# Kernel optimization log

Measured on AMD Instinct MI355X. Metric: run time of the kernel, lower is better.

The kernel has to match this reference:

```python
import jax, jax.numpy as jnp
import numpy as np

EPS = 1e-5

def _layernorm(x, g, b):
    mu = jnp.mean(x, axis=-1, keepdims=True)
    var = jnp.mean(jnp.square(x - mu), axis=-1, keepdims=True)
    return (x - mu) * jax.lax.rsqrt(var + EPS) * g + b

def setup_inputs() -> dict:
    key = jax.random.key(0)
    ks = jax.random.split(key, 12)
    B, S, D, F = 2, 2048, 1024, 4096
    w = lambda k, shp: jax.random.normal(k, shp, dtype=jnp.float32) * 0.02
    return {
        "x":  jax.random.normal(ks[0], (B, S, D), dtype=jnp.float32),
        "Wq": w(ks[1], (D, D)), "bq": jnp.zeros((D,), jnp.float32),
        "Wk": w(ks[2], (D, D)), "bk": jnp.zeros((D,), jnp.float32),
        "Wv": w(ks[3], (D, D)), "bv": jnp.zeros((D,), jnp.float32),
        "W1": w(ks[4], (F, D)), "b1": jnp.zeros((F,), jnp.float32),
        "W2": w(ks[5], (D, F)), "b2": jnp.zeros((D,), jnp.float32),
        "g1": jnp.ones((D,), jnp.float32), "beta1": jnp.zeros((D,), jnp.float32),
        "g2": jnp.ones((D,), jnp.float32), "beta2": jnp.zeros((D,), jnp.float32),
    }

def reference(x, Wq, bq, Wk, bk, Wv, bv, W1, b1, W2, b2, g1, beta1, g2, beta2):
    B, S, D = x.shape
    H = 16
    dk = D // H
    # QKV projections (torch nn.Linear: y = x @ W.T + b)
    q = (x @ Wq.T + bq).reshape(B, S, H, dk).transpose(0, 2, 1, 3)  # [B,H,S,dk]
    k = (x @ Wk.T + bk).reshape(B, S, H, dk).transpose(0, 2, 1, 3)
    v = (x @ Wv.T + bv).reshape(B, S, H, dk).transpose(0, 2, 1, 3)
    # naive full attention (no mask, dropout=identity in eval)
    scores = jnp.einsum("bhqd,bhkd->bhqk", q, k) / jnp.sqrt(jnp.float32(dk))
    probs = jax.nn.softmax(scores, axis=-1)
    attn = jnp.einsum("bhqk,bhkd->bhqd", probs, v)  # [B,H,S,dk]
    attn_out = attn.transpose(0, 2, 1, 3).reshape(B, S, D)  # NOTE: no output proj (combine unused in source)
    # residual + LN1
    h = _layernorm(x + attn_out, g1, beta1)
    # FFN: linear2(relu(linear1(h)))
    ffn = jax.nn.relu(h @ W1.T + b1) @ W2.T + b2
    # residual + LN2
    return _layernorm(h + ffn, g2, beta2)
```

## Files before the change

### kernel.cpp

```cpp
#include <hip/hip_runtime.h>
#include <stdint.h>

typedef unsigned short u16;
typedef __bf16 bf16x8 __attribute__((ext_vector_type(8)));
typedef short s16x8 __attribute__((ext_vector_type(8)));
typedef float f32x4 __attribute__((ext_vector_type(4)));

union FragU { s16x8 s; bf16x8 b; uint4 u; };

__device__ __forceinline__ f32x4 mfma_bf16(s16x8 a, s16x8 b, f32x4 c) {
    FragU ua, ub; ua.s = a; ub.s = b;
    return __builtin_amdgcn_mfma_f32_16x16x32_bf16(ua.b, ub.b, c, 0, 0, 0);
}

__device__ __forceinline__ u16 f2bf(float f) {
    uint32_t u = __float_as_uint(f);
    u += 0x7fffu + ((u >> 16) & 1u);
    return (u16)(u >> 16);
}

__device__ __forceinline__ float bf2f(u16 u) {
    return __uint_as_float((uint32_t)u << 16);
}

__device__ __forceinline__ void gload_lds16(const void* g, void* l) {
    __builtin_amdgcn_global_load_lds((__attribute__((address_space(1))) void*)g,
                                     (__attribute__((address_space(3))) void*)l,
                                     16, 0, 0);
}

__device__ __forceinline__ void xcd_swz(int& bx, int& by, int& bz) {
    int nx = gridDim.x, ny = gridDim.y;
    int nwg = nx * ny * gridDim.z;
    int lin = blockIdx.x + nx * (blockIdx.y + ny * blockIdx.z);
    int cpx = nwg >> 3;
    int s = (lin & 7) * cpx + (lin >> 3);
    bx = s % nx; s /= nx;
    by = s % ny; bz = s / ny;
}

__global__ void k_cast(const float* __restrict__ in, u16* __restrict__ out, int n4) {
    int i = blockIdx.x * blockDim.x + threadIdx.x;
    int stride = gridDim.x * blockDim.x;
    for (; i < n4; i += stride) {
        float4 v = ((const float4*)in)[i];
        u16 us[4] = {f2bf(v.x), f2bf(v.y), f2bf(v.z), f2bf(v.w)};
        *(uint2*)(out + (size_t)i * 4) = *(uint2*)us;
    }
}

template<int RELU, int OUTMODE>
__device__ __forceinline__ void gemm_body(
    const u16* __restrict__ A, const u16* __restrict__ W,
    const float* __restrict__ bias, void* __restrict__ Cout,
    int M, int N, int K, int row0, int col0, int kbeg, int kend)
{
    __shared__ __align__(16) u16 As[128 * 64];
    __shared__ __align__(16) u16 Bs[128 * 64];

    const int tid  = threadIdx.x;
    const int wid  = tid >> 6;
    const int lane = tid & 63;
    const int g    = lane >> 4;
    const int cc   = lane & 15;
    const int wr   = wid >> 1;
    const int wc   = wid & 1;

    f32x4 zero = {0.f, 0.f, 0.f, 0.f};
    f32x4 acc[4][4];
#pragma unroll
    for (int i = 0; i < 4; i++)
#pragma unroll
        for (int j = 0; j < 4; j++) acc[i][j] = zero;

    const int srow = tid >> 3;
    const int scol = ((tid & 7) ^ (srow & 7)) * 8;
    const u16* gA0 = A + (size_t)(row0 + srow) * K + scol;
    const u16* gB0 = W + (size_t)(col0 + srow) * K + scol;
    u16* lA0 = &As[wid * 512];
    u16* lB0 = &Bs[wid * 512];

    const int xm = (cc & 7);

    for (int k0 = kbeg; k0 < kend; k0 += 64) {
#pragma unroll
        for (int j = 0; j < 4; j++)
            gload_lds16(gA0 + (size_t)(j * 32) * K + k0, lA0 + j * 2048);
#pragma unroll
        for (int j = 0; j < 4; j++)
            gload_lds16(gB0 + (size_t)(j * 32) * K + k0, lB0 + j * 2048);
        __syncthreads();

#pragma unroll
        for (int h = 0; h < 2; h++) {
            const int slot = ((h * 4 + g) ^ xm) * 8;
            s16x8 af[4], bf[4];
#pragma unroll
            for (int mi = 0; mi < 4; mi++)
                af[mi] = *(const s16x8*)&As[(wr * 64 + mi * 16 + cc) * 64 + slot];
#pragma unroll
            for (int ni = 0; ni < 4; ni++)
                bf[ni] = *(const s16x8*)&Bs[(wc * 64 + ni * 16 + cc) * 64 + slot];
#pragma unroll
            for (int mi = 0; mi < 4; mi++)
#pragma unroll
                for (int ni = 0; ni < 4; ni++)
                    acc[mi][ni] = mfma_bf16(af[mi], bf[ni], acc[mi][ni]);
        }
        __syncthreads();
    }

#pragma unroll
    for (int ni = 0; ni < 4; ni++) {
        int col = col0 + wc * 64 + ni * 16 + cc;
        float bvv = 0.f;
        if (OUTMODE != 2) bvv = bias[col];
        if (OUTMODE == 3) {
            int head = col >> 6, dh = col & 63;
#pragma unroll
            for (int mi = 0; mi < 4; mi++) {
                int row = row0 + wr * 64 + mi * 16 + g * 4;
                int bb = row >> 11, sl = row & 2047;
                u16 us[4];
#pragma unroll
                for (int r = 0; r < 4; r++) us[r] = f2bf(acc[mi][ni][r] + bvv);
                *(uint2*)&((u16*)Cout)[(((size_t)(bb * 16 + head) * 64 + dh) << 11) + sl]
                    = *(uint2*)us;
            }
        } else {
#pragma unroll
            for (int mi = 0; mi < 4; mi++) {
                int row = row0 + wr * 64 + mi * 16 + g * 4;
#pragma unroll
                for (int r = 0; r < 4; r++) {
                    float v = acc[mi][ni][r] + bvv;
                    if (RELU) v = fmaxf(v, 0.f);
                    size_t idx = (size_t)(row + r) * N + col;
                    if (OUTMODE == 0) ((float*)Cout)[idx] = v;
                    else              ((u16*)Cout)[idx] = f2bf(v);
                }
            }
        }
    }
}

__global__ __launch_bounds__(256, 4) void k_gemm_qk(
    const u16* __restrict__ A, const u16* __restrict__ Wq, const u16* __restrict__ Wk,
    const float* __restrict__ bq, const float* __restrict__ bk,
    u16* __restrict__ Q, u16* __restrict__ K, int M, int N, int Kd)
{
    int bx, by, bz; xcd_swz(bx, by, bz);
    const u16* W = (bz == 0) ? Wq : Wk;
    const float* bb = (bz == 0) ? bq : bk;
    u16* out = (bz == 0) ? Q : K;
    gemm_body<0, 1>(A, W, bb, out, M, N, Kd, by * 128, bx * 128, 0, Kd);
}

__global__ __launch_bounds__(256, 4) void k_gemm_vT(
    const u16* __restrict__ A, const u16* __restrict__ Wv, const float* __restrict__ bv,
    u16* __restrict__ Vt, int M, int N, int Kd)
{
    int bx, by, bz; xcd_swz(bx, by, bz);
    gemm_body<0, 3>(A, Wv, bv, Vt, M, N, Kd, by * 128, bx * 128, 0, Kd);
}

__global__ __launch_bounds__(256, 4) void k_gemm_relu_bf16(
    const u16* __restrict__ A, const u16* __restrict__ W, const float* __restrict__ bias,
    u16* __restrict__ C, int M, int N, int K)
{
    int bx, by, bz; xcd_swz(bx, by, bz);
    gemm_body<1, 1>(A, W, bias, C, M, N, K, by * 128, bx * 128, 0, K);
}

__global__ __launch_bounds__(256, 4) void k_gemm_part(
    const u16* __restrict__ A, const u16* __restrict__ W,
    u16* __restrict__ p0, u16* __restrict__ p1, u16* __restrict__ p2, u16* __restrict__ p3,
    int M, int N, int K)
{
    int bx, by, bz; xcd_swz(bx, by, bz);
    u16* out = (bz == 0) ? p0 : (bz == 1) ? p1 : (bz == 2) ? p2 : p3;
    gemm_body<0, 2>(A, W, nullptr, out, M, N, K, by * 128, bx * 128, bz * 1024, bz * 1024 + 1024);
}

__global__ __launch_bounds__(512, 4) void k_flash(
    const u16* __restrict__ Q, const u16* __restrict__ Kb,
    const u16* __restrict__ Vt, float* __restrict__ O)
{
    constexpr int S = 2048, Dm = 1024, H = 16;
    constexpr int KVB = 128;
    constexpr float qsc = 0.125f * 1.44269504f;
    int bx, by, bz; xcd_swz(bx, by, bz);
    int qt = bx, h = by, b = bz;
    int tid = threadIdx.x, wid = tid >> 6, lane = tid & 63;
    int g = lane >> 4, cc = lane & 15;

    __shared__ __align__(16) u16 Ks[128 * 64];
    __shared__ __align__(16) u16 Vs[64 * 128];

    int q0 = qt * 128 + wid * 16;
    size_t base = (size_t)b * S * Dm + h * 64;

    FragU uq0, uq1, qs0, qs1;
    uq0.s = *(const s16x8*)(Q + base + (size_t)(q0 + cc) * Dm + g * 8);
    uq1.s = *(const s16x8*)(Q + base + (size_t)(q0 + cc) * Dm + 32 + g * 8);
#pragma unroll
    for (int e = 0; e < 8; e++) {
        qs0.b[e] = (__bf16)((float)uq0.b[e] * qsc);
        qs1.b[e] = (__bf16)((float)uq1.b[e] * qsc);
    }
    s16x8 qf0 = qs0.s, qf1 = qs1.s;

    f32x4 minit = {-8.f, -8.f, -8.f, -8.f};
    f32x4 zero = {0.f, 0.f, 0.f, 0.f};
    f32x4 o[4];
#pragma unroll
    for (int t = 0; t < 4; t++) o[t] = zero;
    f32x4 lacc = zero;

    const int krow = tid >> 3;
    const int kcol = ((tid & 7) ^ (krow & 7)) * 8;
    const u16* kSrcBase = Kb + base + (size_t)krow * Dm + kcol;
    u16* kDst0 = &Ks[wid * 512];
    u16* kDst1 = kDst0 + 4096;

    const int vrow = tid >> 3;
    const int vch  = (tid & 7) * 8;
    const int xmv  = (vrow & 7) << 3;
    const int cb0  = ((vch >> 5) << 5) | (((vch >> 4) & 1) << 2) | (((vch >> 2) & 3) << 3);
    const int cb1  = cb0 + 64;
    const u16* vSrcBase = Vt + (size_t)(b * H + h) * 64 * S + (size_t)vrow * S;
    u16* vq0a = &Vs[(vrow * 128 + cb0) ^ xmv];
    u16* vq0b = &Vs[(vrow * 128 + cb0 + 8) ^ xmv];
    u16* vq1a = &Vs[(vrow * 128 + cb1) ^ xmv];
    u16* vq1b = &Vs[(vrow * 128 + cb1 + 8) ^ xmv];

    s16x8 vpre0 = *(const s16x8*)(vSrcBase + vch);
    s16x8 vpre1 = *(const s16x8*)(vSrcBase + 64 + vch);

    const int xm = cc & 7;

    for (int kv0 = 0; kv0 < S; kv0 += KVB) {
        __syncthreads();
        gload_lds16(kSrcBase + (size_t)kv0 * Dm,        kDst0);
        gload_lds16(kSrcBase + (size_t)(kv0 + 64) * Dm, kDst1);
        {
            FragU a0, a1; a0.s = vpre0; a1.s = vpre1;
            *(uint2*)vq0a = make_uint2(a0.u.x, a0.u.y);
            *(uint2*)vq0b = make_uint2(a0.u.z, a0.u.w);
            *(uint2*)vq1a = make_uint2(a1.u.x, a1.u.y);
            *(uint2*)vq1b = make_uint2(a1.u.z, a1.u.w);
        }
        __syncthreads();
        if (kv0 + KVB < S) {
            vpre0 = *(const s16x8*)(vSrcBase + kv0 + KVB + vch);
            vpre1 = *(const s16x8*)(vSrcBase + kv0 + KVB + 64 + vch);
        }

        f32x4 sacc[8];
#pragma unroll
        for (int t = 0; t < 8; t++) sacc[t] = minit;
        __builtin_amdgcn_s_setprio(1);
#pragma unroll
        for (int t = 0; t < 8; t++) {
            const u16* kr = &Ks[(t * 16 + cc) * 64];
            s16x8 kf0 = *(const s16x8*)(kr + ((0 + g) ^ xm) * 8);
            s16x8 kf1 = *(const s16x8*)(kr + ((4 + g) ^ xm) * 8);
            sacc[t] = mfma_bf16(kf0, qf0, sacc[t]);
            sacc[t] = mfma_bf16(kf1, qf1, sacc[t]);
        }
        __builtin_amdgcn_s_setprio(0);

        FragU pb[4];
#pragma unroll
        for (int t = 0; t < 8; t++)
#pragma unroll
            for (int r = 0; r < 4; r++) {
                float pv = __builtin_amdgcn_exp2f(sacc[t][r]);
                lacc[r] += pv;
                pb[t >> 1].b[(t & 1) * 4 + r] = (__bf16)pv;
            }

        __builtin_amdgcn_s_setprio(1);
#pragma unroll
        for (int td = 0; td < 4; td++) {
            const int rb = (td * 16 + cc) * 128;
#pragma unroll
            for (int kk = 0; kk < 4; kk++) {
                s16x8 vf = *(const s16x8*)&Vs[(rb + kk * 32 + g * 8) ^ (xm << 3)];
                o[td] = mfma_bf16(vf, pb[kk].s, o[td]);
            }
        }
        __builtin_amdgcn_s_setprio(0);
    }

    float l_run = (lacc[0] + lacc[1]) + (lacc[2] + lacc[3]);
    l_run += __shfl_xor(l_run, 16, 64);
    l_run += __shfl_xor(l_run, 32, 64);
    float inv = 1.f / l_run;
#pragma unroll
    for (int td = 0; td < 4; td++) {
        float4 st = {o[td][0] * inv, o[td][1] * inv, o[td][2] * inv, o[td][3] * inv};
        *(float4*)&O[(size_t)(b * S + q0 + cc) * Dm + h * 64 + td * 16 + g * 4] = st;
    }
}

__global__ __launch_bounds__(256) void k_ln1(
    const float* __restrict__ A, const float* __restrict__ B,
    const float* __restrict__ gw, const float* __restrict__ bw,
    u16* __restrict__ outb)
{
    constexpr int D = 1024;
    int row = blockIdx.x;
    int t = threadIdx.x;
    int lane = t & 63, wid = t >> 6;
    float4 va = ((const float4*)(A + (size_t)row * D))[t];
    float4 vb = ((const float4*)(B + (size_t)row * D))[t];
    float v0 = va.x + vb.x, v1 = va.y + vb.y, v2 = va.z + vb.z, v3 = va.w + vb.w;
    float sum = v0 + v1 + v2 + v3;
    float sq  = v0 * v0 + v1 * v1 + v2 * v2 + v3 * v3;
#pragma unroll
    for (int off = 1; off < 64; off <<= 1) {
        sum += __shfl_xor(sum, off, 64);
        sq  += __shfl_xor(sq,  off, 64);
    }
    __shared__ float s1[4], s2[4];
    if (lane == 0) { s1[wid] = sum; s2[wid] = sq; }
    __syncthreads();
    sum = s1[0] + s1[1] + s1[2] + s1[3];
    sq  = s2[0] + s2[1] + s2[2] + s2[3];
    float mu  = sum * (1.f / D);
    float var = sq * (1.f / D) - mu * mu;
    float rs  = rsqrtf(var + 1e-5f);
    float4 gv = ((const float4*)gw)[t];
    float4 bv = ((const float4*)bw)[t];
    u16 us[4] = {f2bf((v0 - mu) * rs * gv.x + bv.x),
                 f2bf((v1 - mu) * rs * gv.y + bv.y),
                 f2bf((v2 - mu) * rs * gv.z + bv.z),
                 f2bf((v3 - mu) * rs * gv.w + bv.w)};
    *(uint2*)(outb + (size_t)row * D + t * 4) = *(uint2*)us;
}

__global__ __launch_bounds__(256) void k_ln2(
    const u16* __restrict__ A,
    const u16* __restrict__ p0, const u16* __restrict__ p1,
    const u16* __restrict__ p2, const u16* __restrict__ p3,
    const float* __restrict__ bias,
    const float* __restrict__ gw, const float* __restrict__ bw,
    float* __restrict__ outf)
{
    constexpr int D = 1024;
    int row = blockIdx.x;
    int t = threadIdx.x;
    int lane = t & 63, wid = t >> 6;
    size_t idx = (size_t)row * D + t * 4;
    uint2 ha = *(const uint2*)(A + idx);
    float4 bb = ((const float4*)bias)[t];
    float v0 = bf2f((u16)ha.x)         + bb.x;
    float v1 = bf2f((u16)(ha.x >> 16)) + bb.y;
    float v2 = bf2f((u16)ha.y)         + bb.z;
    float v3 = bf2f((u16)(ha.y >> 16)) + bb.w;
    const u16* ps[4] = {p0, p1, p2, p3};
#pragma unroll
    for (int pi = 0; pi < 4; pi++) {
        uint2 q = *(const uint2*)(ps[pi] + idx);
        v0 += bf2f((u16)q.x);
        v1 += bf2f((u16)(q.x >> 16));
        v2 += bf2f((u16)q.y);
        v3 += bf2f((u16)(q.y >> 16));
    }
    float sum = v0 + v1 + v2 + v3;
    float sq  = v0 * v0 + v1 * v1 + v2 * v2 + v3 * v3;
#pragma unroll
    for (int off = 1; off < 64; off <<= 1) {
        sum += __shfl_xor(sum, off, 64);
        sq  += __shfl_xor(sq,  off, 64);
    }
    __shared__ float s1[4], s2[4];
    if (lane == 0) { s1[wid] = sum; s2[wid] = sq; }
    __syncthreads();
    sum = s1[0] + s1[1] + s1[2] + s1[3];
    sq  = s2[0] + s2[1] + s2[2] + s2[3];
    float mu  = sum * (1.f / D);
    float var = sq * (1.f / D) - mu * mu;
    float rs  = rsqrtf(var + 1e-5f);
    float4 gv = ((const float4*)gw)[t];
    float4 bv = ((const float4*)bw)[t];
    float4 yo = {(v0 - mu) * rs * gv.x + bv.x,
                 (v1 - mu) * rs * gv.y + bv.y,
                 (v2 - mu) * rs * gv.z + bv.z,
                 (v3 - mu) * rs * gv.w + bv.w};
    ((float4*)(outf + (size_t)row * D))[t] = yo;
}

extern "C" void kernel_launch(void* const* d_in, const int* in_sizes, int n_in,
                              void* d_out, int out_size, void* d_ws, size_t ws_size,
                              hipStream_t stream)
{
    constexpr int B = 2, S = 2048, D = 1024, F = 4096, H = 16;
    constexpr int M = B * S;
    const float* x   = (const float*)d_in[0];
    const float* Wq  = (const float*)d_in[1];
    const float* bq  = (const float*)d_in[2];
    const float* Wk  = (const float*)d_in[3];
    const float* bk  = (const float*)d_in[4];
    const float* Wv  = (const float*)d_in[5];
    const float* bv  = (const float*)d_in[6];
    const float* W1  = (const float*)d_in[7];
    const float* b1  = (const float*)d_in[8];
    const float* W2  = (const float*)d_in[9];
    const float* b2  = (const float*)d_in[10];
    const float* g1  = (const float*)d_in[11];
    const float* be1 = (const float*)d_in[12];
    const float* g2  = (const float*)d_in[13];
    const float* be2 = (const float*)d_in[14];
    float* out = (float*)d_out;

    char* ws = (char*)d_ws;
    size_t off = 0;
    auto alloc = [&](size_t bytes) {
        void* p = ws + off;
        off += (bytes + 255) & ~(size_t)255;
        return p;
    };
    u16* xb   = (u16*)alloc((size_t)M * D * 2);
    u16* wqb  = (u16*)alloc((size_t)D * D * 2);
    u16* wkb  = (u16*)alloc((size_t)D * D * 2);
    u16* wvb  = (u16*)alloc((size_t)D * D * 2);
    u16* w1b  = (u16*)alloc((size_t)F * D * 2);
    u16* w2b  = (u16*)alloc((size_t)D * F * 2);
    u16* Qb   = (u16*)alloc((size_t)M * D * 2);
    u16* Kbf  = (u16*)alloc((size_t)M * D * 2);
    u16* Vtb  = (u16*)alloc((size_t)M * D * 2);
    u16* ffn1 = (u16*)alloc((size_t)M * F * 2);
    float* attn = (float*)alloc((size_t)M * D * 4);
    u16* hb     = (u16*)alloc((size_t)M * D * 2);
    u16* p0 = xb;
    u16* p1 = w1b;
    u16* p2 = (u16*)attn;
    u16* p3 = ((u16*)attn) + (size_t)M * D;

    dim3 blk(256);
    k_cast<<<dim3(512), blk, 0, stream>>>(x,  xb,  M * D / 4);
    k_cast<<<dim3(256), blk, 0, stream>>>(Wq, wqb, D * D / 4);
    k_cast<<<dim3(256), blk, 0, stream>>>(Wk, wkb, D * D / 4);
    k_cast<<<dim3(256), blk, 0, stream>>>(Wv, wvb, D * D / 4);
    k_cast<<<dim3(512), blk, 0, stream>>>(W1, w1b, F * D / 4);
    k_cast<<<dim3(512), blk, 0, stream>>>(W2, w2b, D * F / 4);

    k_gemm_qk<<<dim3(D / 128, M / 128, 2), blk, 0, stream>>>(
        xb, wqb, wkb, bq, bk, Qb, Kbf, M, D, D);
    k_gemm_vT<<<dim3(D / 128, M / 128), blk, 0, stream>>>(
        xb, wvb, bv, Vtb, M, D, D);
    k_flash<<<dim3(S / 128, H, B), dim3(512), 0, stream>>>(Qb, Kbf, Vtb, attn);
    k_ln1<<<dim3(M), blk, 0, stream>>>(x, attn, g1, be1, hb);
    k_gemm_relu_bf16<<<dim3(F / 128, M / 128), blk, 0, stream>>>(hb, w1b, b1, ffn1, M, F, D);
    k_gemm_part<<<dim3(D / 128, M / 128, 4), blk, 0, stream>>>(
        ffn1, w2b, p0, p1, p2, p3, M, D, F);
    k_ln2<<<dim3(M), blk, 0, stream>>>(hb, p0, p1, p2, p3, b2, g2, be2, out);
}
```

Before: 209.7 us.

## Double-buffer K tiles in flash attention and merge QKV projection launches

The flash-attention kernel now keeps two K tile buffers in LDS. It prefetches the next K tile with direct global-to-LDS loads while the current tile is being computed, and uses explicit vmcnt/lgkmcnt waits and raw barriers instead of two __syncthreads per iteration. The V prefetch for the next tile moves to the end of the iteration. Separately, the Q/K and V^T projection GEMMs are merged into one launch with a z-dimension of 3, which removes a kernel launch and gives a single larger grid. The changes cost extra LDS, which may lower occupancy, and depend on hand-placed waitcnt counts being correct.

```diff
diff --git a/kernel.cpp b/kernel.cpp
--- a/kernel.cpp
+++ b/kernel.cpp
@@ -144,24 +144,19 @@
     }
 }
 
-__global__ __launch_bounds__(256, 4) void k_gemm_qk(
+__global__ __launch_bounds__(256, 4) void k_gemm_qkv(
     const u16* __restrict__ A, const u16* __restrict__ Wq, const u16* __restrict__ Wk,
-    const float* __restrict__ bq, const float* __restrict__ bk,
-    u16* __restrict__ Q, u16* __restrict__ K, int M, int N, int Kd)
+    const u16* __restrict__ Wv, const float* __restrict__ bq, const float* __restrict__ bk,
+    const float* __restrict__ bv, u16* __restrict__ Q, u16* __restrict__ K,
+    u16* __restrict__ Vt, int M, int N, int Kd)
 {
     int bx, by, bz; xcd_swz(bx, by, bz);
-    const u16* W = (bz == 0) ? Wq : Wk;
-    const float* bb = (bz == 0) ? bq : bk;
-    u16* out = (bz == 0) ? Q : K;
-    gemm_body<0, 1>(A, W, bb, out, M, N, Kd, by * 128, bx * 128, 0, Kd);
-}
-
-__global__ __launch_bounds__(256, 4) void k_gemm_vT(
-    const u16* __restrict__ A, const u16* __restrict__ Wv, const float* __restrict__ bv,
-    u16* __restrict__ Vt, int M, int N, int Kd)
-{
-    int bx, by, bz; xcd_swz(bx, by, bz);
-    gemm_body<0, 3>(A, Wv, bv, Vt, M, N, Kd, by * 128, bx * 128, 0, Kd);
+    if (bz == 0)
+        gemm_body<0, 1>(A, Wq, bq, Q,  M, N, Kd, by * 128, bx * 128, 0, Kd);
+    else if (bz == 1)
+        gemm_body<0, 1>(A, Wk, bk, K,  M, N, Kd, by * 128, bx * 128, 0, Kd);
+    else
+        gemm_body<0, 3>(A, Wv, bv, Vt, M, N, Kd, by * 128, bx * 128, 0, Kd);
 }
 
 __global__ __launch_bounds__(256, 4) void k_gemm_relu_bf16(
@@ -187,14 +182,14 @@
     const u16* __restrict__ Vt, float* __restrict__ O)
 {
     constexpr int S = 2048, Dm = 1024, H = 16;
-    constexpr int KVB = 128;
+    constexpr int KVB = 128, NT = S / KVB;
     constexpr float qsc = 0.125f * 1.44269504f;
     int bx, by, bz; xcd_swz(bx, by, bz);
     int qt = bx, h = by, b = bz;
     int tid = threadIdx.x, wid = tid >> 6, lane = tid & 63;
     int g = lane >> 4, cc = lane & 15;
 
-    __shared__ __align__(16) u16 Ks[128 * 64];
+    __shared__ __align__(16) u16 Ks[2][128 * 64];
     __shared__ __align__(16) u16 Vs[64 * 128];
 
     int q0 = qt * 128 + wid * 16;
@@ -220,8 +215,7 @@
     const int krow = tid >> 3;
     const int kcol = ((tid & 7) ^ (krow & 7)) * 8;
     const u16* kSrcBase = Kb + base + (size_t)krow * Dm + kcol;
-    u16* kDst0 = &Ks[wid * 512];
-    u16* kDst1 = kDst0 + 4096;
+    const int kOff = wid * 512;
 
     const int vrow = tid >> 3;
     const int vch  = (tid & 7) * 8;
@@ -234,15 +228,23 @@
     u16* vq1a = &Vs[(vrow * 128 + cb1) ^ xmv];
     u16* vq1b = &Vs[(vrow * 128 + cb1 + 8) ^ xmv];
 
+    const int xm = cc & 7;
+
+    gload_lds16(kSrcBase,                   &Ks[0][kOff]);
+    gload_lds16(kSrcBase + (size_t)64 * Dm, &Ks[0][kOff + 4096]);
+    __builtin_amdgcn_sched_barrier(0);
     s16x8 vpre0 = *(const s16x8*)(vSrcBase + vch);
     s16x8 vpre1 = *(const s16x8*)(vSrcBase + 64 + vch);
-
-    const int xm = cc & 7;
-
-    for (int kv0 = 0; kv0 < S; kv0 += KVB) {
-        __syncthreads();
-        gload_lds16(kSrcBase + (size_t)kv0 * Dm,        kDst0);
-        gload_lds16(kSrcBase + (size_t)(kv0 + 64) * Dm, kDst1);
+    __builtin_amdgcn_sched_barrier(0);
+
+    for (int it = 0; it < NT; ++it) {
+        const int cur = it & 1;
+        const int kv0 = it * KVB;
+
+        asm volatile("s_waitcnt vmcnt(2)" ::: "memory");
+        __builtin_amdgcn_s_barrier();
+        __builtin_amdgcn_sched_barrier(0);
+
         {
             FragU a0, a1; a0.s = vpre0; a1.s = vpre1;
             *(uint2*)vq0a = make_uint2(a0.u.x, a0.u.y);
@@ -250,19 +252,24 @@
             *(uint2*)vq1a = make_uint2(a1.u.x, a1.u.y);
             *(uint2*)vq1b = make_uint2(a1.u.z, a1.u.w);
         }
-        __syncthreads();
-        if (kv0 + KVB < S) {
-            vpre0 = *(const s16x8*)(vSrcBase + kv0 + KVB + vch);
-            vpre1 = *(const s16x8*)(vSrcBase + kv0 + KVB + 64 + vch);
-        }
-
+        __builtin_amdgcn_sched_barrier(0);
+        if (it + 1 < NT) {
+            gload_lds16(kSrcBase + (size_t)(kv0 + KVB) * Dm,      &Ks[cur ^ 1][kOff]);
+            gload_lds16(kSrcBase + (size_t)(kv0 + KVB + 64) * Dm, &Ks[cur ^ 1][kOff + 4096]);
+        }
+        __builtin_amdgcn_sched_barrier(0);
+        asm volatile("s_waitcnt lgkmcnt(0)" ::: "memory");
+        __builtin_amdgcn_s_barrier();
+        __builtin_amdgcn_sched_barrier(0);
+
+        const u16* Kc = Ks[cur];
         f32x4 sacc[8];
 #pragma unroll
         for (int t = 0; t < 8; t++) sacc[t] = minit;
         __builtin_amdgcn_s_setprio(1);
 #pragma unroll
         for (int t = 0; t < 8; t++) {
-            const u16* kr = &Ks[(t * 16 + cc) * 64];
+            const u16* kr = &Kc[(t * 16 + cc) * 64];
             s16x8 kf0 = *(const s16x8*)(kr + ((0 + g) ^ xm) * 8);
             s16x8 kf1 = *(const s16x8*)(kr + ((4 + g) ^ xm) * 8);
             sacc[t] = mfma_bf16(kf0, qf0, sacc[t]);
@@ -291,6 +298,12 @@
             }
         }
         __builtin_amdgcn_s_setprio(0);
+
+        if (it + 1 < NT) {
+            vpre0 = *(const s16x8*)(vSrcBase + kv0 + KVB + vch);
+            vpre1 = *(const s16x8*)(vSrcBase + kv0 + KVB + 64 + vch);
+        }
+        __builtin_amdgcn_sched_barrier(0);
     }
 
     float l_run = (lacc[0] + lacc[1]) + (lacc[2] + lacc[3]);
@@ -447,10 +460,8 @@
     k_cast<<<dim3(512), blk, 0, stream>>>(W1, w1b, F * D / 4);
     k_cast<<<dim3(512), blk, 0, stream>>>(W2, w2b, D * F / 4);
 
-    k_gemm_qk<<<dim3(D / 128, M / 128, 2), blk, 0, stream>>>(
-        xb, wqb, wkb, bq, bk, Qb, Kbf, M, D, D);
-    k_gemm_vT<<<dim3(D / 128, M / 128), blk, 0, stream>>>(
-        xb, wvb, bv, Vtb, M, D, D);
+    k_gemm_qkv<<<dim3(D / 128, M / 128, 3), blk, 0, stream>>>(
+        xb, wqb, wkb, wvb, bq, bk, bv, Qb, Kbf, Vtb, M, D, D);
     k_flash<<<dim3(S / 128, H, B), dim3(512), 0, stream>>>(Qb, Kbf, Vtb, attn);
     k_ln1<<<dim3(M), blk, 0, stream>>>(x, attn, g1, be1, hb);
     k_gemm_relu_bf16<<<dim3(F / 128, M / 128), blk, 0, stream>>>(hb, w1b, b1, ffn1, M, F, D);
```

New measurement: 210.6 us. Within noise of the previous version (+0.4%).
